# Performance work log

Measured on AMD Instinct MI355X. Metric: run time of the kernel, lower is better.

## Reference

```python
import jax, jax.numpy as jnp
import numpy as np

# Fixed rotation angles (radians) standing in for IMAGE_ROTATE_DETECTOR_ANGLES[dataset]
ANGLES = [-0.5236, -0.2618, 0.0, 0.2618, 0.5236]
SHIFT_PIXELS = [1, 2, 3, 4, 5]  # shift_pixels_one_direction


def _shift_mats(H, W):
    # Direction enum iteration order: up, down, left, right; 'right' gets extra 0.
    mats = []
    for direction in ('up', 'down', 'left', 'right'):
        ps = SHIFT_PIXELS + ([0] if direction == 'right' else [])
        for p in ps:
            if direction == 'left':
                tx, ty = p, 0
            elif direction == 'right':
                tx, ty = -p, 0
            elif direction == 'up':
                tx, ty = 0, p
            else:  # down
                tx, ty = 0, -p
            mats.append([[1.0, 0.0, tx / float(W - 1)], [0.0, 1.0, ty / float(H - 1)]])
    return np.asarray(mats, dtype=np.float32)  # (S, 2, 3)


def _rotate_mats():
    mats = [[[np.cos(a), np.sin(a), 0.0], [-np.sin(a), np.cos(a), 0.0]] for a in ANGLES]
    return np.asarray(mats, dtype=np.float32)  # (R, 2, 3)


def _affine_grid(theta, H, W):
    # torch F.affine_grid with align_corners=True
    xs = jnp.linspace(-1.0, 1.0, W)
    ys = jnp.linspace(-1.0, 1.0, H)
    gx, gy = jnp.meshgrid(xs, ys)                       # (H, W)
    base = jnp.stack([gx, gy, jnp.ones_like(gx)], -1)   # (H, W, 3)
    return jnp.einsum('hwk,nik->nhwi', base, theta)     # (N, H, W, 2) -> (x, y)


def _grid_sample(img, grid):
    # torch F.grid_sample, bilinear, zero padding, align_corners=True
    N, C, H, W = img.shape
    ix = (grid[..., 0] + 1.0) * (W - 1) * 0.5           # (N, H, W)
    iy = (grid[..., 1] + 1.0) * (H - 1) * 0.5
    x0 = jnp.floor(ix)
    y0 = jnp.floor(iy)
    wx = ix - x0
    wy = iy - y0

    def corner(xi, yi, w):
        valid = (xi >= 0) & (xi <= W - 1) & (yi >= 0) & (yi <= H - 1)
        xc = jnp.clip(xi, 0, W - 1).astype(jnp.int32)
        yc = jnp.clip(yi, 0, H - 1).astype(jnp.int32)
        v = jax.vmap(lambda im, yy, xx: im[:, yy, xx])(img, yc, xc)  # (N, C, H, W)
        return v * (w * valid)[:, None]

    return (corner(x0, y0, (1 - wx) * (1 - wy))
            + corner(x0 + 1, y0, wx * (1 - wy))
            + corner(x0, y0 + 1, (1 - wx) * wy)
            + corner(x0 + 1, y0 + 1, wx * wy))


def setup_inputs() -> dict:
    key = jax.random.key(0)
    xs = jax.random.uniform(key, (4, 224, 224, 3), dtype=jnp.float32)
    return {"xs": xs}


def reference(xs):
    B, H, W, C = xs.shape
    x = jnp.transpose(xs, (0, 3, 1, 2))                 # (B, C, H, W)

    # Stage 1: pixel shifts. Output order = (shift s, image b) flattened as s*B + b.
    S_mats = jnp.asarray(_shift_mats(H, W))             # (S, 2, 3)
    S = S_mats.shape[0]
    x1 = jnp.broadcast_to(x[None], (S, B, C, H, W)).reshape(S * B, C, H, W)
    g1 = _affine_grid(jnp.repeat(S_mats, B, axis=0), H, W)
    x1 = _grid_sample(x1, g1)                           # (S*B, C, H, W)

    # Stage 2: rotations of the shifted batch. Order = (angle r, n) flattened as r*(S*B) + n.
    R_mats = jnp.asarray(_rotate_mats())                # (R, 2, 3)
    R = R_mats.shape[0]
    x2 = jnp.broadcast_to(x1[None], (R, S * B, C, H, W)).reshape(R * S * B, C, H, W)
    g2 = _affine_grid(jnp.repeat(R_mats, S * B, axis=0), H, W)
    out = _grid_sample(x2, g2)                          # (R*S*B, C, H, W)

    out = jnp.transpose(out, (0, 2, 3, 1))              # NHWC
    return out.reshape(R * S, B, H, W, C)
```

## Files before the change

### kernel.cpp

```cpp
#include <hip/hip_runtime.h>

namespace {

constexpr int H = 224, W = 224, B = 4, S = 21, R = 5;
constexpr int HW = H * W;

__constant__ float c_sin[5] = {-0.5000010604f, -0.2588196365f, 0.0f,
                                0.2588196365f,  0.5000010604f};
__constant__ float c_cos[5] = { 0.8660247916f,  0.9659256678f, 1.0f,
                                0.9659256678f,  0.8660247916f};

struct alignas(4) f3 { float x, y, z; };

__device__ __forceinline__ float vIn(int x) {
    return ((unsigned)x < (unsigned)W) ? 1.0f : 0.0f;
}
__device__ __forceinline__ int clampW(int x) {
    return min(max(x, 0), W - 1);
}

__global__ __launch_bounds__(256) void fused_shift_rotate(
    const float* __restrict__ xs, float* __restrict__ out) {
    int pix = blockIdx.x * 256 + threadIdx.x;
    int h = pix / W;
    int w = pix - h * W;
    int b = blockIdx.y;
    int r = blockIdx.z;

    float sr = c_sin[r], cr = c_cos[r];
    const float cx = 0.5f * (W - 1);
    float dx = (float)w - cx;
    float dy = (float)h - cx;
    float ix = fmaf(dy, sr, fmaf(dx, cr, cx));
    float iy = fmaf(dy, cr, fmaf(-dx, sr, cx));

    float x0f = floorf(ix), y0f = floorf(iy);
    int x0 = (int)x0f, y0 = (int)y0f;
    float wx = ix - x0f, wy = iy - y0f;
    float wxl = 1.0f - wx, wyl = 1.0f - wy;

    float vx0 = vIn(x0), vx1 = vIn(x0 + 1);
    float vy0 = vIn(y0), vy1 = vIn(y0 + 1);
    float rwy0 = wyl * vy0, rwy1 = wy * vy1;
    float cwx0 = wxl * vx0, cwx1 = wx * vx1;

    const float* img = xs + (size_t)b * (HW * 3);
    size_t obase = ((size_t)(r * S) * B + b) * (size_t)(HW * 3) + (size_t)pix * 3;
    constexpr size_t splane = (size_t)B * HW * 3;

    {
        float Hb[2][8][3];
        const float* r0 = img + clampW(y0) * (W * 3);
        const float* r1 = img + clampW(y0 + 1) * (W * 3);
        #pragma unroll
        for (int j = 0; j < 8; ++j) {
            int xc = clampW(x0 - 3 + j) * 3;
            const f3 t0 = *(const f3*)(r0 + xc);
            const f3 t1 = *(const f3*)(r1 + xc);
            Hb[0][j][0] = t0.x; Hb[0][j][1] = t0.y; Hb[0][j][2] = t0.z;
            Hb[1][j][0] = t1.x; Hb[1][j][1] = t1.y; Hb[1][j][2] = t1.z;
        }
        constexpr int tx_tab[11] = {1, 2, 3, 4, 5, -1, -2, -3, -4, -5, 0};
        #pragma unroll
        for (int k = 0; k < 11; ++k) {
            const int tx = tx_tab[k];
            const int s = 10 + k;
            float a[3];
            if (tx & 1) {
                const int j = ((tx - 1) >> 1) + 3;
                int xb = x0 + ((tx - 1) >> 1);
                float cw0 = 0.5f * wxl * vx0 * vIn(xb);
                float cw1 = 0.5f * (wxl * vx0 + wx * vx1) * vIn(xb + 1);
                float cw2 = 0.5f * wx * vx1 * vIn(xb + 2);
                #pragma unroll
                for (int c = 0; c < 3; ++c)
                    a[c] = rwy0 * (cw0 * Hb[0][j][c] + cw1 * Hb[0][j + 1][c] + cw2 * Hb[0][j + 2][c])
                         + rwy1 * (cw0 * Hb[1][j][c] + cw1 * Hb[1][j + 1][c] + cw2 * Hb[1][j + 2][c]);
            } else {
                const int sx = tx >> 1;
                const int j = sx + 3;
                float ax0 = cwx0 * vIn(x0 + sx);
                float ax1 = cwx1 * vIn(x0 + 1 + sx);
                #pragma unroll
                for (int c = 0; c < 3; ++c)
                    a[c] = rwy0 * (ax0 * Hb[0][j][c] + ax1 * Hb[0][j + 1][c])
                         + rwy1 * (ax0 * Hb[1][j][c] + ax1 * Hb[1][j + 1][c]);
            }
            f3* op = (f3*)(out + obase + (size_t)s * splane);
            f3 v; v.x = a[0]; v.y = a[1]; v.z = a[2];
            *op = v;
        }
    }

    {
        float Vb[8][2][3];
        int xc0 = clampW(x0) * 3, xc1 = clampW(x0 + 1) * 3;
        #pragma unroll
        for (int i = 0; i < 8; ++i) {
            const float* rr = img + clampW(y0 - 3 + i) * (W * 3);
            const f3 t0 = *(const f3*)(rr + xc0);
            const f3 t1 = *(const f3*)(rr + xc1);
            Vb[i][0][0] = t0.x; Vb[i][0][1] = t0.y; Vb[i][0][2] = t0.z;
            Vb[i][1][0] = t1.x; Vb[i][1][1] = t1.y; Vb[i][1][2] = t1.z;
        }
        constexpr int ty_tab[10] = {1, 2, 3, 4, 5, -1, -2, -3, -4, -5};
        #pragma unroll
        for (int k = 0; k < 10; ++k) {
            const int ty = ty_tab[k];
            const int s = k;
            float a[3];
            if (ty & 1) {
                const int i = ((ty - 1) >> 1) + 3;
                int yb = y0 + ((ty - 1) >> 1);
                float rw0 = 0.5f * wyl * vy0 * vIn(yb);
                float rw1 = 0.5f * (wyl * vy0 + wy * vy1) * vIn(yb + 1);
                float rw2 = 0.5f * wy * vy1 * vIn(yb + 2);
                #pragma unroll
                for (int c = 0; c < 3; ++c)
                    a[c] = cwx0 * (rw0 * Vb[i][0][c] + rw1 * Vb[i + 1][0][c] + rw2 * Vb[i + 2][0][c])
                         + cwx1 * (rw0 * Vb[i][1][c] + rw1 * Vb[i + 1][1][c] + rw2 * Vb[i + 2][1][c]);
            } else {
                const int sy = ty >> 1;
                const int i = sy + 3;
                float ay0 = rwy0 * vIn(y0 + sy);
                float ay1 = rwy1 * vIn(y0 + 1 + sy);
                #pragma unroll
                for (int c = 0; c < 3; ++c)
                    a[c] = cwx0 * (ay0 * Vb[i][0][c] + ay1 * Vb[i + 1][0][c])
                         + cwx1 * (ay0 * Vb[i][1][c] + ay1 * Vb[i + 1][1][c]);
            }
            f3* op = (f3*)(out + obase + (size_t)s * splane);
            f3 v; v.x = a[0]; v.y = a[1]; v.z = a[2];
            *op = v;
        }
    }
}

}

extern "C" void kernel_launch(void* const* d_in, const int* in_sizes, int n_in,
                              void* d_out, int out_size, void* d_ws, size_t ws_size,
                              hipStream_t stream) {
    const float* xs = (const float*)d_in[0];
    float* out = (float*)d_out;
    dim3 grid(HW / 256, B, R);
    fused_shift_rotate<<<grid, dim3(256), 0, stream>>>(xs, out);
}
```

Measured before the change: 247.9 us.

## Stage rotated source windows in LDS with 2D pixel tiles

```diff
diff --git a/kernel.cpp b/kernel.cpp
--- a/kernel.cpp
+++ b/kernel.cpp
@@ -4,6 +4,13 @@
 
 constexpr int H = 224, W = 224, B = 4, S = 21, R = 5;
 constexpr int HW = H * W;
+
+constexpr int TW = 32, TH = 8;
+constexpr int GX = W / TW;
+constexpr int GY = H / TH;
+constexpr int WINW = 40, WINH = 32;
+constexpr int LROW = WINW * 3;
+constexpr int LSIZE = WINH * LROW;
 
 __constant__ float c_sin[5] = {-0.5000010604f, -0.2588196365f, 0.0f,
                                 0.2588196365f,  0.5000010604f};
@@ -15,48 +22,71 @@
 __device__ __forceinline__ float vIn(int x) {
     return ((unsigned)x < (unsigned)W) ? 1.0f : 0.0f;
 }
-__device__ __forceinline__ int clampW(int x) {
-    return min(max(x, 0), W - 1);
-}
 
-__global__ __launch_bounds__(256) void fused_shift_rotate(
+__global__ __launch_bounds__(256) void fused_shift_rotate_lds(
     const float* __restrict__ xs, float* __restrict__ out) {
-    int pix = blockIdx.x * 256 + threadIdx.x;
-    int h = pix / W;
-    int w = pix - h * W;
-    int b = blockIdx.y;
-    int r = blockIdx.z;
+    __shared__ float lds[LSIZE];
+    const int tid = threadIdx.x;
+    const int tile = blockIdx.x;
+    const int tx0 = (tile % GX) * TW;
+    const int ty0 = (tile / GX) * TH;
+    const int b = blockIdx.y;
+    const int r = blockIdx.z;
 
-    float sr = c_sin[r], cr = c_cos[r];
+    const float sr = c_sin[r], cr = c_cos[r];
     const float cx = 0.5f * (W - 1);
-    float dx = (float)w - cx;
-    float dy = (float)h - cx;
-    float ix = fmaf(dy, sr, fmaf(dx, cr, cx));
-    float iy = fmaf(dy, cr, fmaf(-dx, sr, cx));
 
-    float x0f = floorf(ix), y0f = floorf(iy);
-    int x0 = (int)x0f, y0 = (int)y0f;
-    float wx = ix - x0f, wy = iy - y0f;
-    float wxl = 1.0f - wx, wyl = 1.0f - wy;
-
-    float vx0 = vIn(x0), vx1 = vIn(x0 + 1);
-    float vy0 = vIn(y0), vy1 = vIn(y0 + 1);
-    float rwy0 = wyl * vy0, rwy1 = wy * vy1;
-    float cwx0 = wxl * vx0, cwx1 = wx * vx1;
+    const float dxs = (float)tx0 - cx, dxe = (float)(tx0 + TW - 1) - cx;
+    const float dys = (float)ty0 - cx, dye = (float)(ty0 + TH - 1) - cx;
+    const float ixmin = cx + dxs * cr + fminf(dys * sr, dye * sr);
+    const float iymin = cx + fminf(-dxs * sr, -dxe * sr) + dys * cr;
+    const int cmin = min(max((int)floorf(ixmin) - 3, 0), W - WINW);
+    const int rmin = min(max((int)floorf(iymin) - 3, 0), H - WINH);
 
     const float* img = xs + (size_t)b * (HW * 3);
+    const float* gsrc = img + rmin * (W * 3) + cmin * 3;
+    #pragma unroll
+    for (int k = 0; k < LSIZE / 256; ++k) {
+        int idx = tid + k * 256;
+        int row = idx / LROW;
+        int f = idx - row * LROW;
+        lds[idx] = gsrc[row * (W * 3) + f];
+    }
+    __syncthreads();
+
+    const int wpx = tx0 + (tid & (TW - 1));
+    const int hpx = ty0 + (tid >> 5);
+    const float dx = (float)wpx - cx;
+    const float dy = (float)hpx - cx;
+    const float ix = fmaf(dy, sr, fmaf(dx, cr, cx));
+    const float iy = fmaf(dy, cr, fmaf(-dx, sr, cx));
+
+    const float x0f = floorf(ix), y0f = floorf(iy);
+    const int x0 = (int)x0f, y0 = (int)y0f;
+    const float wx = ix - x0f, wy = iy - y0f;
+    const float wxl = 1.0f - wx, wyl = 1.0f - wy;
+
+    const float vx0 = vIn(x0), vx1 = vIn(x0 + 1);
+    const float vy0 = vIn(y0), vy1 = vIn(y0 + 1);
+    const float rwy0 = wyl * vy0, rwy1 = wy * vy1;
+    const float cwx0 = wxl * vx0, cwx1 = wx * vx1;
+
+    const int pix = hpx * W + wpx;
     size_t obase = ((size_t)(r * S) * B + b) * (size_t)(HW * 3) + (size_t)pix * 3;
     constexpr size_t splane = (size_t)B * HW * 3;
 
+    auto lcol = [&](int g) { int l = g - cmin; return min(max(l, 0), WINW - 1); };
+    auto lrow = [&](int g) { int l = g - rmin; return min(max(l, 0), WINH - 1); };
+
     {
         float Hb[2][8][3];
-        const float* r0 = img + clampW(y0) * (W * 3);
-        const float* r1 = img + clampW(y0 + 1) * (W * 3);
+        const float* R0 = &lds[lrow(y0) * LROW];
+        const float* R1 = &lds[lrow(y0 + 1) * LROW];
         #pragma unroll
         for (int j = 0; j < 8; ++j) {
-            int xc = clampW(x0 - 3 + j) * 3;
-            const f3 t0 = *(const f3*)(r0 + xc);
-            const f3 t1 = *(const f3*)(r1 + xc);
+            int xc = lcol(x0 - 3 + j) * 3;
+            const f3 t0 = *(const f3*)(R0 + xc);
+            const f3 t1 = *(const f3*)(R1 + xc);
             Hb[0][j][0] = t0.x; Hb[0][j][1] = t0.y; Hb[0][j][2] = t0.z;
             Hb[1][j][0] = t1.x; Hb[1][j][1] = t1.y; Hb[1][j][2] = t1.z;
         }
@@ -94,12 +124,12 @@
 
     {
         float Vb[8][2][3];
-        int xc0 = clampW(x0) * 3, xc1 = clampW(x0 + 1) * 3;
+        int xc0 = lcol(x0) * 3, xc1 = lcol(x0 + 1) * 3;
         #pragma unroll
         for (int i = 0; i < 8; ++i) {
-            const float* rr = img + clampW(y0 - 3 + i) * (W * 3);
-            const f3 t0 = *(const f3*)(rr + xc0);
-            const f3 t1 = *(const f3*)(rr + xc1);
+            const float* RR = &lds[lrow(y0 - 3 + i) * LROW];
+            const f3 t0 = *(const f3*)(RR + xc0);
+            const f3 t1 = *(const f3*)(RR + xc1);
             Vb[i][0][0] = t0.x; Vb[i][0][1] = t0.y; Vb[i][0][2] = t0.z;
             Vb[i][1][0] = t1.x; Vb[i][1][1] = t1.y; Vb[i][1][2] = t1.z;
         }
@@ -143,6 +173,6 @@
                               hipStream_t stream) {
     const float* xs = (const float*)d_in[0];
     float* out = (float*)d_out;
-    dim3 grid(HW / 256, B, R);
-    fused_shift_rotate<<<grid, dim3(256), 0, stream>>>(xs, out);
+    dim3 grid(GX * GY, B, R);
+    fused_shift_rotate_lds<<<grid, dim3(256), 0, stream>>>(xs, out);
 }
```

Result: no change. 243.3 us (-1.9%).
